# Optimization experiments

Measured on AMD Instinct MI355X. Metric: run time of the kernel, lower is better.

## Reference

```python
import jax, jax.numpy as jnp
import numpy as np

T, B, I, H = 2048, 64, 256, 256

def setup_inputs() -> dict:
    key = jax.random.key(0)
    k_x, k_wih, k_whh = jax.random.split(key, 3)
    x = jax.random.normal(k_x, (T, B, I), dtype=jnp.float32)
    h0 = jnp.zeros((1, B, H), dtype=jnp.float32)
    # nn.RNN weight_ih_l0 init: U(-1/sqrt(H), 1/sqrt(H)); shape [H, I]
    bound = 1.0 / np.sqrt(H)
    W_ih = jax.random.uniform(k_wih, (H, I), minval=-bound, maxval=bound, dtype=jnp.float32)
    # IndRNN recurrent weight: diagonal vector, U(-1, 1); biases are zeroed.
    w_hh = jax.random.uniform(k_whh, (H,), minval=-1.0, maxval=1.0, dtype=jnp.float32)
    return {"x": x, "h0": h0, "W_ih": W_ih, "w_hh": w_hh}

def reference(x, h0, W_ih, w_hh):
    # Precompute the input projection for all timesteps (the only GEMM):
    # [T, B, H] = x @ W_ih^T  (biases are zero)
    xW = jnp.einsum('tbi,hi->tbh', x, W_ih)

    def step(h, xw_t):
        # IndRNN: diagonal recurrence -> elementwise multiply instead of matmul
        h_new = jax.nn.relu(xw_t + h * w_hh)
        return h_new, h_new

    h_last, outputs = jax.lax.scan(step, h0[0], xW)
    return outputs, h_last[None]  # ([T,B,H], [1,B,H]) matching nn.RNN
```

## Files before the change

kernel.cpp:

```cpp
#include <hip/hip_runtime.h>

typedef short v8s __attribute__((ext_vector_type(8)));
typedef float v4f __attribute__((ext_vector_type(4)));

#define BH 16384
#define TBH 33554432
#define SEG 16
#define SEGT 128
#define SCAN_TILE 128
#define NTILE 16

__device__ __forceinline__ ushort f2bf(float f) {
  uint u = __float_as_uint(f);
  u += 0x7FFF + ((u >> 16) & 1);
  return (ushort)(u >> 16);
}

__global__ __launch_bounds__(512) void indrnn_gemm(
    const float* __restrict__ A,
    const float* __restrict__ W,
    ushort* __restrict__ C)
{
  __shared__ ushort As[128 * 72];
  __shared__ ushort Bs[256 * 72];

  const int tid  = threadIdx.x;
  const int lane = tid & 63;
  const int wid  = tid >> 6;
  const int wm   = wid >> 2;
  const int wn   = wid & 3;
  const int m0   = blockIdx.x * 128;

  const int l15 = lane & 15;
  const int lhi = lane >> 4;

  v4f acc[4][4] = {};

  for (int kc = 0; kc < 4; ++kc) {
    #pragma unroll
    for (int j = 0; j < 4; ++j) {
      int f    = j * 512 + tid;
      int row  = f >> 4;
      int colf = f & 15;
      const float4 a4 = *(const float4*)(A + ((size_t)(m0 + row) << 8) + kc * 64 + colf * 4);
      ushort4 b4 = make_ushort4(f2bf(a4.x), f2bf(a4.y), f2bf(a4.z), f2bf(a4.w));
      *(ushort4*)(As + row * 72 + colf * 4) = b4;
    }
    #pragma unroll
    for (int j = 0; j < 8; ++j) {
      int f    = j * 512 + tid;
      int row  = f >> 4;
      int colf = f & 15;
      const float4 a4 = *(const float4*)(W + ((size_t)row << 8) + kc * 64 + colf * 4);
      ushort4 b4 = make_ushort4(f2bf(a4.x), f2bf(a4.y), f2bf(a4.z), f2bf(a4.w));
      *(ushort4*)(Bs + row * 72 + colf * 4) = b4;
    }
    __syncthreads();

    #pragma unroll
    for (int kk = 0; kk < 2; ++kk) {
      const int koff = kk * 32 + lhi * 8;
      v8s af[4], bf[4];
      #pragma unroll
      for (int mt = 0; mt < 4; ++mt)
        af[mt] = *(const v8s*)(As + (wm * 64 + mt * 16 + l15) * 72 + koff);
      #pragma unroll
      for (int nt = 0; nt < 4; ++nt)
        bf[nt] = *(const v8s*)(Bs + (wn * 64 + nt * 16 + l15) * 72 + koff);
      #pragma unroll
      for (int mt = 0; mt < 4; ++mt)
        #pragma unroll
        for (int nt = 0; nt < 4; ++nt)
          acc[mt][nt] = __builtin_amdgcn_mfma_f32_16x16x32_bf16(af[mt], bf[nt], acc[mt][nt], 0, 0, 0);
    }
    __syncthreads();
  }

  #pragma unroll
  for (int mt = 0; mt < 4; ++mt) {
    #pragma unroll
    for (int nt = 0; nt < 4; ++nt) {
      #pragma unroll
      for (int r = 0; r < 4; ++r) {
        int row = m0 + wm * 64 + mt * 16 + lhi * 4 + r;
        int col = wn * 64 + nt * 16 + l15;
        C[((size_t)row << 8) + col] = f2bf(acc[mt][nt][r]);
      }
    }
  }
}

__global__ __launch_bounds__(256) void indrnn_seg(
    const ushort* __restrict__ xw,
    const float* __restrict__ w_hh,
    float4* __restrict__ fn)
{
  const int chgrp = blockIdx.x & 63;
  const int seg   = blockIdx.x >> 6;
  const int ch    = chgrp * 256 + threadIdx.x;
  const float w   = w_hh[ch & 255];
  const ushort* px = xw + (size_t)seg * SEGT * BH + ch;

  float p = 1.0f, a = 0.0f, lo = -3.402823466e38f, hi = 3.402823466e38f;

  uint b0[16], b1[16];
  auto ldb = [&](uint (&buf)[16], int kb) {
    const ushort* q = px + (size_t)kb * 16 * BH;
    #pragma unroll
    for (int j = 0; j < 16; ++j) buf[j] = q[(size_t)j * BH];
  };
  auto comp = [&](uint (&buf)[16]) {
    #pragma unroll
    for (int j = 0; j < 16; ++j) {
      float xv = __uint_as_float(buf[j] << 16);
      float A = fmaf(w, lo, xv);
      float B = fmaf(w, hi, xv);
      lo = fmaxf(0.0f, fminf(A, B));
      hi = fmaxf(0.0f, fmaxf(A, B));
      a  = fmaf(w, a, xv);
      p *= w;
    }
  };

  ldb(b0, 0); ldb(b1, 1);
  for (int kb = 0; kb < 8; kb += 2) {
    comp(b0); if (kb + 2 < 8) ldb(b0, kb + 2);
    comp(b1); if (kb + 3 < 8) ldb(b1, kb + 3);
  }
  fn[(size_t)seg * BH + ch] = make_float4(p, a, lo, hi);
}

__global__ __launch_bounds__(256) void indrnn_fix(
    const ushort* __restrict__ xw,
    const float* __restrict__ h0,
    const float* __restrict__ w_hh,
    const float4* __restrict__ fn,
    float* __restrict__ out)
{
  const int chgrp = blockIdx.x & 63;
  const int seg   = blockIdx.x >> 6;
  const int ch    = chgrp * 256 + threadIdx.x;
  const float w   = w_hh[ch & 255];

  float h = h0[ch];
  for (int s = 0; s < seg; ++s) {
    const float4 F = fn[(size_t)s * BH + ch];
    h = fminf(fmaxf(fmaf(F.x, h, F.y), F.z), F.w);
  }

  const ushort* px = xw + (size_t)seg * SEGT * BH + ch;
  float*        po = out + (size_t)seg * SEGT * BH + ch;

  uint b0[16], b1[16];
  auto ldb = [&](uint (&buf)[16], int kb) {
    const ushort* q = px + (size_t)kb * 16 * BH;
    #pragma unroll
    for (int j = 0; j < 16; ++j) buf[j] = q[(size_t)j * BH];
  };
  auto cp = [&](uint (&buf)[16], int kb) {
    float* o = po + (size_t)kb * 16 * BH;
    #pragma unroll
    for (int j = 0; j < 16; ++j) {
      float xv = __uint_as_float(buf[j] << 16);
      h = fmaxf(fmaf(h, w, xv), 0.0f);
      o[(size_t)j * BH] = h;
    }
  };

  ldb(b0, 0); ldb(b1, 1);
  for (int kb = 0; kb < 8; kb += 2) {
    cp(b0, kb);     if (kb + 2 < 8) ldb(b0, kb + 2);
    cp(b1, kb + 1); if (kb + 3 < 8) ldb(b1, kb + 3);
  }

  if (seg == SEG - 1) out[(size_t)TBH + ch] = h;
}

__global__ __launch_bounds__(128) void indrnn_scan(
    const ushort* __restrict__ xw,
    const float* __restrict__ h0,
    const float* __restrict__ w_hh,
    float* __restrict__ out)
{
  __shared__ __align__(16) ushort tile[3][SCAN_TILE * 64];

  const int lane = threadIdx.x & 63;
  const int wv   = threadIdx.x >> 6;
  const int ch0  = blockIdx.x * 64;
  const int ch   = ch0 + lane;

  const size_t psrc0 = (size_t)(lane >> 3) * BH + (size_t)ch0 + ((lane & 7) << 3);

  auto stage = [&](int ti) {
    const ushort* src = xw + (size_t)ti * SCAN_TILE * BH + psrc0;
    ushort* dst = &tile[ti % 3][0];
    #pragma unroll
    for (int j = 0; j < 16; ++j) {
      __builtin_amdgcn_global_load_lds(
          (const float*)(src + (size_t)j * 8 * BH),
          (float*)(dst + j * 512), 16, 0, 0);
    }
  };

  float h = 0.0f, w = 0.0f;
  if (wv == 0) {
    h = h0[ch];
    w = w_hh[ch & 255];
  } else {
    stage(0);
    stage(1);
    asm volatile("s_waitcnt vmcnt(16)" ::: "memory");
  }
  asm volatile("" ::: "memory");
  __builtin_amdgcn_s_barrier();
  __builtin_amdgcn_sched_barrier(0);

  for (int i = 0; i < NTILE; ++i) {
    if (wv == 0) {
      const ushort* tp = &tile[i % 3][lane];
      float* po = out + (size_t)i * SCAN_TILE * BH + ch;
      #pragma unroll
      for (int t = 0; t < SCAN_TILE; t += 16) {
        ushort v[16];
        #pragma unroll
        for (int j = 0; j < 16; ++j) v[j] = tp[(t + j) * 64];
        #pragma unroll
        for (int j = 0; j < 16; ++j) {
          float xv = __uint_as_float((uint)v[j] << 16);
          h = fmaxf(fmaf(h, w, xv), 0.0f);
          po[(size_t)(t + j) * BH] = h;
        }
      }
    } else {
      if (i + 2 < NTILE) {
        stage(i + 2);
        asm volatile("s_waitcnt vmcnt(16)" ::: "memory");
      } else {
        asm volatile("s_waitcnt vmcnt(0)" ::: "memory");
      }
    }
    asm volatile("" ::: "memory");
    __builtin_amdgcn_s_barrier();
    __builtin_amdgcn_sched_barrier(0);
  }

  if (wv == 0) out[(size_t)TBH + ch] = h;
}

extern "C" void kernel_launch(void* const* d_in, const int* in_sizes, int n_in,
                              void* d_out, int out_size, void* d_ws, size_t ws_size,
                              hipStream_t stream) {
  const float* x    = (const float*)d_in[0];
  const float* h0   = (const float*)d_in[1];
  const float* W_ih = (const float*)d_in[2];
  const float* w_hh = (const float*)d_in[3];
  float* out = (float*)d_out;
  ushort* xw = (ushort*)d_ws;

  indrnn_gemm<<<dim3(1024), dim3(512), 0, stream>>>(x, W_ih, xw);

  const size_t need = (64ull << 20) + (size_t)SEG * BH * sizeof(float4);
  if (ws_size >= need) {
    float4* fn = (float4*)((char*)d_ws + (64ull << 20));
    indrnn_seg<<<dim3(1024), dim3(256), 0, stream>>>(xw, w_hh, fn);
    indrnn_fix<<<dim3(1024), dim3(256), 0, stream>>>(xw, h0, w_hh, fn, out);
  } else {
    indrnn_scan<<<dim3(256), dim3(128), 0, stream>>>(xw, h0, w_hh, out);
  }
}
```

Measured before the change: 286.1 us.

## Pre-convert W to swizzled bf16 and stream A via direct global-to-LDS loads

Adds a small kernel that converts W_ih once per call to bf16 in an XOR-swizzled layout. The GEMM is reworked into 64-row tiles with 256 threads, launched on more blocks. A and the bf16 weights are now loaded straight into LDS with global_load_lds, and A is packed to bf16 from LDS with v_cvt_pk_bf16_f32 during fragment assembly. The aim is to cut register staging and conversion on the load path, avoid LDS bank conflicts and raise occupancy, at the cost of one extra launch and redundant A conversion by each wave. The old GEMM is kept as a fallback for the small-workspace path.

```diff
diff --git a/kernel.cpp b/kernel.cpp
--- a/kernel.cpp
+++ b/kernel.cpp
@@ -16,64 +16,97 @@
   return (ushort)(u >> 16);
 }
 
-__global__ __launch_bounds__(512) void indrnn_gemm(
+__device__ __forceinline__ uint pkbf2(float a, float b) {
+  uint r;
+  asm("v_cvt_pk_bf16_f32 %0, %1, %2" : "=v"(r) : "v"(a), "v"(b));
+  return r;
+}
+
+union frag_u { uint u[4]; v8s s; };
+
+__global__ __launch_bounds__(256) void indrnn_w2bf(
+    const float* __restrict__ W, ushort* __restrict__ Wbf)
+{
+  const int g   = blockIdx.x * 256 + threadIdx.x;
+  const int kc  = g >> 11;
+  const int rem = g & 2047;
+  const int row = rem >> 3;
+  const int sp  = rem & 7;
+  const int slog = sp ^ (row & 7);
+  const float* src = W + row * 256 + kc * 64 + slog * 8;
+  const float4 f0 = *(const float4*)src;
+  const float4 f1 = *(const float4*)(src + 4);
+  uint4 o;
+  o.x = pkbf2(f0.x, f0.y); o.y = pkbf2(f0.z, f0.w);
+  o.z = pkbf2(f1.x, f1.y); o.w = pkbf2(f1.z, f1.w);
+  *(uint4*)(Wbf + (size_t)g * 8) = o;
+}
+
+__global__ __launch_bounds__(256, 3) void indrnn_gemm(
     const float* __restrict__ A,
-    const float* __restrict__ W,
+    const ushort* __restrict__ Wbf,
     ushort* __restrict__ C)
 {
-  __shared__ ushort As[128 * 72];
-  __shared__ ushort Bs[256 * 72];
-
-  const int tid  = threadIdx.x;
-  const int lane = tid & 63;
-  const int wid  = tid >> 6;
-  const int wm   = wid >> 2;
-  const int wn   = wid & 3;
-  const int m0   = blockIdx.x * 128;
-
-  const int l15 = lane & 15;
-  const int lhi = lane >> 4;
+  __shared__ __align__(16) float  Af[4096];
+  __shared__ __align__(16) ushort Bs[16384];
+
+  const int tid   = threadIdx.x;
+  const int lane  = tid & 63;
+  const int wn    = tid >> 6;
+  const int l15   = lane & 15;
+  const int lhi   = lane >> 4;
+  const int m0    = blockIdx.x * 64;
+  const int bflat = tid & 192;
 
   v4f acc[4][4] = {};
 
   for (int kc = 0; kc < 4; ++kc) {
+    if (kc) __syncthreads();
+
     #pragma unroll
     for (int j = 0; j < 4; ++j) {
-      int f    = j * 512 + tid;
-      int row  = f >> 4;
-      int colf = f & 15;
-      const float4 a4 = *(const float4*)(A + ((size_t)(m0 + row) << 8) + kc * 64 + colf * 4);
-      ushort4 b4 = make_ushort4(f2bf(a4.x), f2bf(a4.y), f2bf(a4.z), f2bf(a4.w));
-      *(ushort4*)(As + row * 72 + colf * 4) = b4;
+      const int bf_ = j * 256 + bflat;
+      const int fl  = bf_ + lane;
+      const int row = fl >> 4;
+      const int sl  = fl & 15;
+      const float* src = A + ((size_t)(m0 + row) << 8) + kc * 64 + ((sl ^ (row & 7)) << 2);
+      __builtin_amdgcn_global_load_lds(src, &Af[bf_ << 2], 16, 0, 0);
     }
     #pragma unroll
     for (int j = 0; j < 8; ++j) {
-      int f    = j * 512 + tid;
-      int row  = f >> 4;
-      int colf = f & 15;
-      const float4 a4 = *(const float4*)(W + ((size_t)row << 8) + kc * 64 + colf * 4);
-      ushort4 b4 = make_ushort4(f2bf(a4.x), f2bf(a4.y), f2bf(a4.z), f2bf(a4.w));
-      *(ushort4*)(Bs + row * 72 + colf * 4) = b4;
-    }
+      const int bf_ = j * 256 + bflat;
+      const int fl  = bf_ + lane;
+      __builtin_amdgcn_global_load_lds(
+          (const float*)(Wbf + (size_t)kc * 16384 + (size_t)fl * 8),
+          (float*)(Bs + (size_t)bf_ * 8), 16, 0, 0);
+    }
+    asm volatile("s_waitcnt vmcnt(0)" ::: "memory");
     __syncthreads();
 
     #pragma unroll
     for (int kk = 0; kk < 2; ++kk) {
-      const int koff = kk * 32 + lhi * 8;
-      v8s af[4], bf[4];
-      #pragma unroll
-      for (int mt = 0; mt < 4; ++mt)
-        af[mt] = *(const v8s*)(As + (wm * 64 + mt * 16 + l15) * 72 + koff);
-      #pragma unroll
-      for (int nt = 0; nt < 4; ++nt)
-        bf[nt] = *(const v8s*)(Bs + (wn * 64 + nt * 16 + l15) * 72 + koff);
-      #pragma unroll
-      for (int mt = 0; mt < 4; ++mt)
+      v8s bfr[4];
+      #pragma unroll
+      for (int nt = 0; nt < 4; ++nt) {
+        const int row = wn * 64 + nt * 16 + l15;
+        const int sp  = (kk * 4 + lhi) ^ (row & 7);
+        bfr[nt] = *(const v8s*)((const char*)Bs + row * 128 + sp * 16);
+      }
+      #pragma unroll
+      for (int mt = 0; mt < 4; ++mt) {
+        const int row = mt * 16 + l15;
+        const int s0  = kk * 8 + lhi * 2;
+        const char* base = (const char*)Af + row * 256;
+        const float4 lo = *(const float4*)(base + ((s0 ^ (row & 7)) << 4));
+        const float4 hi = *(const float4*)(base + (((s0 + 1) ^ (row & 7)) << 4));
+        frag_u t;
+        t.u[0] = pkbf2(lo.x, lo.y); t.u[1] = pkbf2(lo.z, lo.w);
+        t.u[2] = pkbf2(hi.x, hi.y); t.u[3] = pkbf2(hi.z, hi.w);
         #pragma unroll
         for (int nt = 0; nt < 4; ++nt)
-          acc[mt][nt] = __builtin_amdgcn_mfma_f32_16x16x32_bf16(af[mt], bf[nt], acc[mt][nt], 0, 0, 0);
-    }
-    __syncthreads();
+          acc[mt][nt] = __builtin_amdgcn_mfma_f32_16x16x32_bf16(t.s, bfr[nt], acc[mt][nt], 0, 0, 0);
+      }
+    }
   }
 
   #pragma unroll
@@ -82,7 +115,7 @@
     for (int nt = 0; nt < 4; ++nt) {
       #pragma unroll
       for (int r = 0; r < 4; ++r) {
-        int row = m0 + wm * 64 + mt * 16 + lhi * 4 + r;
+        int row = m0 + mt * 16 + lhi * 4 + r;
         int col = wn * 64 + nt * 16 + l15;
         C[((size_t)row << 8) + col] = f2bf(acc[mt][nt][r]);
       }
@@ -174,6 +207,77 @@
   }
 
   if (seg == SEG - 1) out[(size_t)TBH + ch] = h;
+}
+
+__global__ __launch_bounds__(512) void indrnn_gemm_fb(
+    const float* __restrict__ A,
+    const float* __restrict__ W,
+    ushort* __restrict__ C)
+{
+  __shared__ ushort As[128 * 72];
+  __shared__ ushort Bs[256 * 72];
+
+  const int tid  = threadIdx.x;
+  const int lane = tid & 63;
+  const int wid  = tid >> 6;
+  const int wm   = wid >> 2;
+  const int wn   = wid & 3;
+  const int m0   = blockIdx.x * 128;
+  const int l15 = lane & 15;
+  const int lhi = lane >> 4;
+
+  v4f acc[4][4] = {};
+
+  for (int kc = 0; kc < 4; ++kc) {
+    #pragma unroll
+    for (int j = 0; j < 4; ++j) {
+      int f    = j * 512 + tid;
+      int row  = f >> 4;
+      int colf = f & 15;
+      const float4 a4 = *(const float4*)(A + ((size_t)(m0 + row) << 8) + kc * 64 + colf * 4);
+      ushort4 b4 = make_ushort4(f2bf(a4.x), f2bf(a4.y), f2bf(a4.z), f2bf(a4.w));
+      *(ushort4*)(As + row * 72 + colf * 4) = b4;
+    }
+    #pragma unroll
+    for (int j = 0; j < 8; ++j) {
+      int f    = j * 512 + tid;
+      int row  = f >> 4;
+      int colf = f & 15;
+      const float4 a4 = *(const float4*)(W + ((size_t)row << 8) + kc * 64 + colf * 4);
+      ushort4 b4 = make_ushort4(f2bf(a4.x), f2bf(a4.y), f2bf(a4.z), f2bf(a4.w));
+      *(ushort4*)(Bs + row * 72 + colf * 4) = b4;
+    }
+    __syncthreads();
+
+    #pragma unroll
+    for (int kk = 0; kk < 2; ++kk) {
+      const int koff = kk * 32 + lhi * 8;
+      v8s af[4], bf[4];
+      #pragma unroll
+      for (int mt = 0; mt < 4; ++mt)
+        af[mt] = *(const v8s*)(As + (wm * 64 + mt * 16 + l15) * 72 + koff);
+      #pragma unroll
+      for (int nt = 0; nt < 4; ++nt)
+        bf[nt] = *(const v8s*)(Bs + (wn * 64 + nt * 16 + l15) * 72 + koff);
+      #pragma unroll
+      for (int mt = 0; mt < 4; ++mt)
+        #pragma unroll
+        for (int nt = 0; nt < 4; ++nt)
+          acc[mt][nt] = __builtin_amdgcn_mfma_f32_16x16x32_bf16(af[mt], bf[nt], acc[mt][nt], 0, 0, 0);
+    }
+    __syncthreads();
+  }
+
+  #pragma unroll
+  for (int mt = 0; mt < 4; ++mt)
+    #pragma unroll
+    for (int nt = 0; nt < 4; ++nt)
+      #pragma unroll
+      for (int r = 0; r < 4; ++r) {
+        int row = m0 + wm * 64 + mt * 16 + lhi * 4 + r;
+        int col = wn * 64 + nt * 16 + l15;
+        C[((size_t)row << 8) + col] = f2bf(acc[mt][nt][r]);
+      }
 }
 
 __global__ __launch_bounds__(128) void indrnn_scan(
@@ -257,14 +361,19 @@
   float* out = (float*)d_out;
   ushort* xw = (ushort*)d_ws;
 
-  indrnn_gemm<<<dim3(1024), dim3(512), 0, stream>>>(x, W_ih, xw);
-
-  const size_t need = (64ull << 20) + (size_t)SEG * BH * sizeof(float4);
+  const size_t off_fn = 64ull << 20;
+  const size_t off_wb = off_fn + (size_t)SEG * BH * sizeof(float4);
+  const size_t need   = off_wb + 131072;
+
   if (ws_size >= need) {
-    float4* fn = (float4*)((char*)d_ws + (64ull << 20));
-    indrnn_seg<<<dim3(1024), dim3(256), 0, stream>>>(xw, w_hh, fn);
-    indrnn_fix<<<dim3(1024), dim3(256), 0, stream>>>(xw, h0, w_hh, fn, out);
+    float4* fn  = (float4*)((char*)d_ws + off_fn);
+    ushort* wbf = (ushort*)((char*)d_ws + off_wb);
+    indrnn_w2bf<<<dim3(32),   dim3(256), 0, stream>>>(W_ih, wbf);
+    indrnn_gemm<<<dim3(2048), dim3(256), 0, stream>>>(x, wbf, xw);
+    indrnn_seg <<<dim3(1024), dim3(256), 0, stream>>>(xw, w_hh, fn);
+    indrnn_fix <<<dim3(1024), dim3(256), 0, stream>>>(xw, h0, w_hh, fn, out);
   } else {
+    indrnn_gemm_fb<<<dim3(1024), dim3(512), 0, stream>>>(x, W_ih, xw);
     indrnn_scan<<<dim3(256), dim3(128), 0, stream>>>(xw, h0, w_hh, out);
   }
 }
```

New measurement: 281.2 us. No clear change (-1.7%).
